# Kernel optimization log

Measured on AMD Instinct MI355X. Metric: run time of the kernel, lower is better.

Reference implementation:

```python
import jax, jax.numpy as jnp
import numpy as np

B, S, D = 4, 4096, 1024
E, I = 8, 2048
CAPACITY = 2
K = max(1, int(S / E * CAPACITY))  # tokens per expert per batch element


def setup_inputs() -> dict:
    key = jax.random.key(0)
    k1, k2, k3, k4, k5 = jax.random.split(key, 5)
    x = jax.random.normal(k1, (B, S, D), dtype=jnp.float32)
    gate_w = jax.random.normal(k2, (D, E), dtype=jnp.float32) * 0.006
    Wg = jax.random.normal(k3, (E, D, I), dtype=jnp.float32) * 0.02
    Wu = jax.random.normal(k4, (E, D, I), dtype=jnp.float32) * 0.02
    Wd = jax.random.normal(k5, (E, I, D), dtype=jnp.float32) * 0.02
    return {"x": x, "gate_w": gate_w, "Wg": Wg, "Wu": Wu, "Wd": Wd}


def reference(x, gate_w, Wg, Wu, Wd):
    # Router: softmax over experts per token, then per-expert top-k tokens.
    logits = jnp.einsum('bsd,de->bse', x, gate_w)          # [B,S,E]
    affinity = jax.nn.softmax(logits, axis=-1)
    affinity_T = jnp.transpose(affinity, (0, 2, 1))        # [B,E,S]
    gating, index = jax.lax.top_k(affinity_T, K)           # [B,E,K]

    # Gather selected tokens for all experts at once: [B,E,K,D]
    b_idx = jnp.arange(x.shape[0])[:, None, None]
    x_sel = x[b_idx, index]

    # Per-expert SwiGLU MLP (grouped GEMMs over the expert axis).
    g = jnp.einsum('bekd,edi->beki', x_sel, Wg)
    u = jnp.einsum('bekd,edi->beki', x_sel, Wu)
    h = jax.nn.silu(g) * u
    out = jnp.einsum('beki,eid->bekd', h, Wd)              # [B,E,K,D]

    # Weighted scatter-add combine back to token positions.
    contrib = out * gating[..., None]
    x_out = jnp.zeros_like(x).at[b_idx, index].add(contrib)
    return x_out
```

## Files before the change

### kernel.cpp

```cpp
#include <hip/hip_runtime.h>

#define B_ 4
#define S_ 4096
#define D_ 1024
#define E_ 8
#define I_ 2048
#define K_ 1024

typedef __attribute__((ext_vector_type(8))) short short8;
typedef __attribute__((ext_vector_type(4))) float f32x4;

__device__ __forceinline__ short f2bf(float f) {
  union { float f; unsigned u; } v; v.f = f;
  unsigned r = v.u + 0x7FFFu + ((v.u >> 16) & 1u);
  return (short)(r >> 16);
}

__device__ __forceinline__ void gload16(const void* g, void* l) {
  __builtin_amdgcn_global_load_lds((const __attribute__((address_space(1))) unsigned int*)g,
                                   (__attribute__((address_space(3))) unsigned int*)l, 16, 0, 0);
}

__global__ __launch_bounds__(256) void router_kernel(const float* __restrict__ x,
                                                     const float* __restrict__ gw,
                                                     double* __restrict__ affD) {
  int wave = threadIdx.x >> 6, lane = threadIdx.x & 63;
  int tok = blockIdx.x * 4 + wave;
  int b = tok >> 12, s = tok & (S_ - 1);
  const float* xr = x + (size_t)tok * D_;
  double acc[E_];
#pragma unroll
  for (int e = 0; e < E_; ++e) acc[e] = 0.0;
#pragma unroll 4
  for (int r = 0; r < 16; ++r) {
    int d = r * 64 + lane;
    float xv = xr[d];
    const float4* g4 = reinterpret_cast<const float4*>(gw + (size_t)d * E_);
    float4 g0 = g4[0], g1 = g4[1];
    acc[0] += (double)xv * g0.x; acc[1] += (double)xv * g0.y;
    acc[2] += (double)xv * g0.z; acc[3] += (double)xv * g0.w;
    acc[4] += (double)xv * g1.x; acc[5] += (double)xv * g1.y;
    acc[6] += (double)xv * g1.z; acc[7] += (double)xv * g1.w;
  }
#pragma unroll
  for (int off = 32; off > 0; off >>= 1) {
#pragma unroll
    for (int e = 0; e < E_; ++e) acc[e] += __shfl_xor(acc[e], off, 64);
  }
  double m = acc[0];
#pragma unroll
  for (int e = 1; e < E_; ++e) m = acc[e] > m ? acc[e] : m;
  double den = 0.0, ex[E_];
#pragma unroll
  for (int e = 0; e < E_; ++e) { ex[e] = exp(acc[e] - m); den += ex[e]; }
  if (lane < E_)
    affD[((size_t)b * E_ + lane) * S_ + s] = ex[lane] / den;
}

__global__ __launch_bounds__(1024) void topk_kernel(const double* __restrict__ affD,
                                                    int* __restrict__ idxArr,
                                                    float* __restrict__ gateArr) {
  __shared__ unsigned long long keys[S_];
  __shared__ int sidx[S_];
  int be = blockIdx.x, tid = threadIdx.x;
  const double* a = affD + (size_t)be * S_;
  for (int t = tid; t < S_; t += 1024) {
    keys[t] = (unsigned long long)__double_as_longlong(a[t]);
    sidx[t] = t;
  }
  __syncthreads();
  for (int k = 2; k <= S_; k <<= 1) {
    for (int j = k >> 1; j > 0; j >>= 1) {
      for (int t = tid; t < S_; t += 1024) {
        int x2 = t ^ j;
        if (x2 > t) {
          unsigned long long ka = keys[t], kb = keys[x2];
          int ia = sidx[t], ib = sidx[x2];
          bool agt = (ka > kb) || (ka == kb && ia < ib);
          bool up = ((t & k) == 0);
          if (up == agt) {
            keys[t] = kb; keys[x2] = ka;
            sidx[t] = ib; sidx[x2] = ia;
          }
        }
      }
      __syncthreads();
    }
  }
  for (int t = tid; t < K_; t += 1024) {
    int p = S_ - 1 - t;
    gateArr[(size_t)be * K_ + t] = (float)__longlong_as_double((long long)keys[p]);
    idxArr[(size_t)be * K_ + t] = sidx[p];
  }
}

__global__ __launch_bounds__(256) void transpose_cvt_kernel(const float* __restrict__ in,
                                                            unsigned short* __restrict__ out,
                                                            int M, int N) {
  __shared__ float t[64][65];
  int e = blockIdx.y;
  int ntn = N >> 6;
  int tm = (blockIdx.x / ntn) << 6;
  int tn = (blockIdx.x % ntn) << 6;
  const float* src = in + (size_t)e * M * N;
  unsigned short* dst = out + (size_t)e * M * N;
  int tid = threadIdx.x;
#pragma unroll
  for (int it = 0; it < 4; ++it) {
    int f = it * 256 + tid;
    int r = f >> 4, c4 = (f & 15) << 2;
    float4 v = *reinterpret_cast<const float4*>(&src[(size_t)(tm + r) * N + tn + c4]);
    t[c4][r] = v.x; t[c4 + 1][r] = v.y; t[c4 + 2][r] = v.z; t[c4 + 3][r] = v.w;
  }
  __syncthreads();
#pragma unroll
  for (int it = 0; it < 4; ++it) {
    int f = it * 256 + tid;
    int rr = f >> 4, c4 = (f & 15) << 2;
    short4 o;
    o.x = f2bf(t[rr][c4]); o.y = f2bf(t[rr][c4 + 1]);
    o.z = f2bf(t[rr][c4 + 2]); o.w = f2bf(t[rr][c4 + 3]);
    *reinterpret_cast<short4*>(&dst[(size_t)(tn + rr) * M + tm + c4]) = o;
  }
}

__global__ __launch_bounds__(256, 2) void mlp1_kernel(
    const float* __restrict__ x, const unsigned short* __restrict__ WgT,
    const unsigned short* __restrict__ WuT, const int* __restrict__ idxArr,
    unsigned short* __restrict__ H, int Ic, int i0) {
  const int Nt = Ic >> 7;
  int bid = blockIdx.x;
  int nt = bid % Nt; bid /= Nt;
  int mt = bid & 7; bid >>= 3;
  int be = bid;
  int b = be >> 3, e = be & 7;

  __shared__ short lsA[128 * 72];
  __shared__ short lsBg[128 * 64];
  __shared__ short lsBu[128 * 64];
  __shared__ int sTok[128];

  int tid = threadIdx.x;
  if (tid < 128) sTok[tid] = idxArr[(size_t)be * K_ + mt * 128 + tid];
  __syncthreads();

  const float* xb = x + (size_t)b * S_ * D_;
  const char* wg2 = (const char*)(WgT + (size_t)e * I_ * D_ + (size_t)(i0 + nt * 128) * D_);
  const char* wu2 = (const char*)(WuT + (size_t)e * I_ * D_ + (size_t)(i0 + nt * 128) * D_);

  int w = tid >> 6, lane = tid & 63;
  int wm = w >> 1, wn = w & 1;
  int lr = lane & 15, lg = lane >> 4;

  f32x4 accg[4][4], accu[4][4];
#pragma unroll
  for (int i = 0; i < 4; ++i)
#pragma unroll
    for (int j = 0; j < 4; ++j) {
      accg[i][j] = (f32x4){0.f, 0.f, 0.f, 0.f};
      accu[i][j] = (f32x4){0.f, 0.f, 0.f, 0.f};
    }

  for (int k0 = 0; k0 < D_; k0 += 64) {
#pragma unroll
    for (int c = 0; c < 4; ++c) {
      int flat = (c * 256 + tid) * 8;
      int row = flat >> 6, col = flat & 63;
      const float* src = xb + (size_t)sTok[row] * D_ + k0 + col;
      float4 f0 = *reinterpret_cast<const float4*>(src);
      float4 f1 = *reinterpret_cast<const float4*>(src + 4);
      short8 t;
      t[0] = f2bf(f0.x); t[1] = f2bf(f0.y); t[2] = f2bf(f0.z); t[3] = f2bf(f0.w);
      t[4] = f2bf(f1.x); t[5] = f2bf(f1.y); t[6] = f2bf(f1.z); t[7] = f2bf(f1.w);
      *reinterpret_cast<short8*>(&lsA[row * 72 + col]) = t;
    }
#pragma unroll
    for (int c = 0; c < 4; ++c) {
      int chunk = c * 4 + w;
      int fb = (chunk * 64 + lane) * 16;
      int row = fb >> 7, colb = fb & 127;
      size_t goff = (size_t)row * (D_ * 2) + (size_t)k0 * 2 + colb;
      gload16(wg2 + goff, (char*)lsBg + chunk * 1024);
      gload16(wu2 + goff, (char*)lsBu + chunk * 1024);
    }
    __syncthreads();
#pragma unroll
    for (int fk = 0; fk < 2; ++fk) {
      short8 af[4], bgf[4], buf[4];
#pragma unroll
      for (int fm = 0; fm < 4; ++fm)
        af[fm] = *reinterpret_cast<short8*>(&lsA[(wm * 64 + fm * 16 + lr) * 72 + fk * 32 + lg * 8]);
#pragma unroll
      for (int fn = 0; fn < 4; ++fn) {
        bgf[fn] = *reinterpret_cast<short8*>(&lsBg[(wn * 64 + fn * 16 + lr) * 64 + fk * 32 + lg * 8]);
        buf[fn] = *reinterpret_cast<short8*>(&lsBu[(wn * 64 + fn * 16 + lr) * 64 + fk * 32 + lg * 8]);
      }
#pragma unroll
      for (int fm = 0; fm < 4; ++fm)
#pragma unroll
        for (int fn = 0; fn < 4; ++fn) {
          accg[fm][fn] = __builtin_amdgcn_mfma_f32_16x16x32_bf16(af[fm], bgf[fn], accg[fm][fn], 0, 0, 0);
          accu[fm][fn] = __builtin_amdgcn_mfma_f32_16x16x32_bf16(af[fm], buf[fn], accu[fm][fn], 0, 0, 0);
        }
    }
    __syncthreads();
  }
  unsigned short* Hbe = H + (size_t)be * K_ * Ic;
#pragma unroll
  for (int fm = 0; fm < 4; ++fm)
#pragma unroll
    for (int fn = 0; fn < 4; ++fn) {
#pragma unroll
      for (int j = 0; j < 4; ++j) {
        float g = accg[fm][fn][j], u = accu[fm][fn][j];
        float h = g / (1.f + __expf(-g)) * u;
        int row = wm * 64 + fm * 16 + lg * 4 + j;
        int col = wn * 64 + fn * 16 + lr;
        Hbe[(size_t)(mt * 128 + row) * Ic + nt * 128 + col] = (unsigned short)f2bf(h);
      }
    }
}

__global__ __launch_bounds__(256, 2) void mlp2_kernel(
    const unsigned short* __restrict__ H, const unsigned short* __restrict__ WdT,
    const int* __restrict__ idxArr, const float* __restrict__ gateArr,
    float* __restrict__ out, int Ic, int i0) {
  int bid = blockIdx.x;
  int nt = bid & 7; bid >>= 3;
  int mt = bid & 7; bid >>= 3;
  int be = bid;
  int b = be >> 3, e = be & 7;

  __shared__ short lsA[128 * 64];
  __shared__ short lsB[128 * 64];
  __shared__ int sTok[128];
  __shared__ float sGate[128];

  int tid = threadIdx.x;
  if (tid < 128) {
    sTok[tid] = idxArr[(size_t)be * K_ + mt * 128 + tid];
    sGate[tid] = gateArr[(size_t)be * K_ + mt * 128 + tid];
  }
  __syncthreads();

  const char* Hbe = (const char*)(H + (size_t)be * K_ * Ic);
  const char* wd2 = (const char*)(WdT + (size_t)e * D_ * I_);

  int w = tid >> 6, lane = tid & 63;
  int wm = w >> 1, wn = w & 1;
  int lr = lane & 15, lg = lane >> 4;

  f32x4 acc[4][4];
#pragma unroll
  for (int i = 0; i < 4; ++i)
#pragma unroll
    for (int j = 0; j < 4; ++j) acc[i][j] = (f32x4){0.f, 0.f, 0.f, 0.f};

  for (int k0 = 0; k0 < Ic; k0 += 64) {
#pragma unroll
    for (int c = 0; c < 4; ++c) {
      int chunk = c * 4 + w;
      int fb = (chunk * 64 + lane) * 16;
      int row = fb >> 7, colb = fb & 127;
      gload16(Hbe + (size_t)(mt * 128 + row) * Ic * 2 + (size_t)k0 * 2 + colb,
              (char*)lsA + chunk * 1024);
      gload16(wd2 + ((size_t)(nt * 128 + row) * I_ + i0 + k0) * 2 + colb,
              (char*)lsB + chunk * 1024);
    }
    __syncthreads();
#pragma unroll
    for (int fk = 0; fk < 2; ++fk) {
      short8 af[4], bf[4];
#pragma unroll
      for (int fm = 0; fm < 4; ++fm)
        af[fm] = *reinterpret_cast<short8*>(&lsA[(wm * 64 + fm * 16 + lr) * 64 + fk * 32 + lg * 8]);
#pragma unroll
      for (int fn = 0; fn < 4; ++fn)
        bf[fn] = *reinterpret_cast<short8*>(&lsB[(wn * 64 + fn * 16 + lr) * 64 + fk * 32 + lg * 8]);
#pragma unroll
      for (int fm = 0; fm < 4; ++fm)
#pragma unroll
        for (int fn = 0; fn < 4; ++fn)
          acc[fm][fn] = __builtin_amdgcn_mfma_f32_16x16x32_bf16(af[fm], bf[fn], acc[fm][fn], 0, 0, 0);
    }
    __syncthreads();
  }
#pragma unroll
  for (int fm = 0; fm < 4; ++fm)
#pragma unroll
    for (int fn = 0; fn < 4; ++fn) {
#pragma unroll
      for (int j = 0; j < 4; ++j) {
        int row = wm * 64 + fm * 16 + lg * 4 + j;
        int col = nt * 128 + wn * 64 + fn * 16 + lr;
        float v = acc[fm][fn][j] * sGate[row];
        atomicAdd(&out[((size_t)b * S_ + sTok[row]) * D_ + col], v);
      }
    }
}

extern "C" void kernel_launch(void* const* d_in, const int* in_sizes, int n_in,
                              void* d_out, int out_size, void* d_ws, size_t ws_size,
                              hipStream_t stream) {
  const float* x  = (const float*)d_in[0];
  const float* gw = (const float*)d_in[1];
  const float* Wg = (const float*)d_in[2];
  const float* Wu = (const float*)d_in[3];
  const float* Wd = (const float*)d_in[4];
  float* out = (float*)d_out;
  char* ws = (char*)d_ws;

  size_t off = 0;
  double* affD = (double*)(ws + off); off += (size_t)B_ * E_ * S_ * sizeof(double);
  int* idxArr = (int*)(ws + off);     off += (size_t)B_ * E_ * K_ * sizeof(int);
  float* gateArr = (float*)(ws + off); off += (size_t)B_ * E_ * K_ * sizeof(float);
  off = (off + 255) & ~(size_t)255;
  unsigned short* WgT = (unsigned short*)(ws + off); off += (size_t)E_ * D_ * I_ * 2;
  unsigned short* WuT = (unsigned short*)(ws + off); off += (size_t)E_ * D_ * I_ * 2;
  unsigned short* WdT = (unsigned short*)(ws + off); off += (size_t)E_ * D_ * I_ * 2;
  off = (off + 255) & ~(size_t)255;
  unsigned short* H = (unsigned short*)(ws + off);
  size_t rem = (ws_size > off) ? (ws_size - off) : 0;

  int Ic = 128;
  for (int c = I_; c >= 128; c >>= 1) {
    if ((size_t)B_ * E_ * K_ * (size_t)c * 2 <= rem) { Ic = c; break; }
  }

  hipMemsetAsync(d_out, 0, (size_t)out_size * sizeof(float), stream);
  router_kernel<<<B_ * S_ / 4, 256, 0, stream>>>(x, gw, affD);
  topk_kernel<<<B_ * E_, 1024, 0, stream>>>(affD, idxArr, gateArr);
  transpose_cvt_kernel<<<dim3((D_ / 64) * (I_ / 64), E_), 256, 0, stream>>>(Wg, WgT, D_, I_);
  transpose_cvt_kernel<<<dim3((D_ / 64) * (I_ / 64), E_), 256, 0, stream>>>(Wu, WuT, D_, I_);
  transpose_cvt_kernel<<<dim3((I_ / 64) * (D_ / 64), E_), 256, 0, stream>>>(Wd, WdT, I_, D_);
  for (int i0 = 0; i0 < I_; i0 += Ic) {
    mlp1_kernel<<<B_ * E_ * 8 * (Ic / 128), 256, 0, stream>>>(x, WgT, WuT, idxArr, H, Ic, i0);
    mlp2_kernel<<<B_ * E_ * 8 * 8, 256, 0, stream>>>(H, WdT, idxArr, gateArr, out, Ic, i0);
  }
}
```

Before: 805.4 us.

## Pre-gather bf16 tokens, swizzle LDS tiles, and remap workgroups across XCDs

Adds a gather kernel that converts the selected tokens to a contiguous bf16 buffer. mlp1 can then load A tiles with direct global-to-LDS loads instead of doing per-iteration fp32 gathers and conversions. Both MLP kernels now use an XOR-swizzled LDS layout in place of padding to avoid bank conflicts, and remap block IDs so neighbouring tiles land on the same XCD for L2 reuse. This costs an extra kernel launch and about 64 MB of workspace, which can shrink the available Ic chunk size.

```diff
diff --git a/kernel.cpp b/kernel.cpp
--- a/kernel.cpp
+++ b/kernel.cpp
@@ -19,6 +19,11 @@
 __device__ __forceinline__ void gload16(const void* g, void* l) {
   __builtin_amdgcn_global_load_lds((const __attribute__((address_space(1))) unsigned int*)g,
                                    (__attribute__((address_space(3))) unsigned int*)l, 16, 0, 0);
+}
+
+__device__ __forceinline__ short8 rdswz(const short* ls, int row, int cb) {
+  int byte = (row << 7) + (cb ^ ((row & 7) << 4));
+  return *reinterpret_cast<const short8*>(reinterpret_cast<const char*>(ls) + byte);
 }
 
 __global__ __launch_bounds__(256) void router_kernel(const float* __restrict__ x,
@@ -124,33 +129,51 @@
   }
 }
 
+__global__ __launch_bounds__(256) void gather_cvt_kernel(const float* __restrict__ x,
+                                                         const int* __restrict__ idxArr,
+                                                         unsigned short* __restrict__ Xsel) {
+  int row = blockIdx.x * 4 + (threadIdx.x >> 6);
+  int lane = threadIdx.x & 63;
+  int b = row >> 13;
+  int tok = idxArr[row];
+  const float* src = x + ((size_t)b * S_ + tok) * D_;
+  unsigned short* dst = Xsel + (size_t)row * D_;
+#pragma unroll
+  for (int it = 0; it < 4; ++it) {
+    int d = it * 256 + lane * 4;
+    float4 v = *reinterpret_cast<const float4*>(src + d);
+    short4 o;
+    o.x = f2bf(v.x); o.y = f2bf(v.y); o.z = f2bf(v.z); o.w = f2bf(v.w);
+    *reinterpret_cast<short4*>(dst + d) = o;
+  }
+}
+
 __global__ __launch_bounds__(256, 2) void mlp1_kernel(
-    const float* __restrict__ x, const unsigned short* __restrict__ WgT,
-    const unsigned short* __restrict__ WuT, const int* __restrict__ idxArr,
-    unsigned short* __restrict__ H, int Ic, int i0) {
+    const unsigned short* __restrict__ Xsel, const unsigned short* __restrict__ WgT,
+    const unsigned short* __restrict__ WuT, unsigned short* __restrict__ H,
+    int Ic, int i0) {
   const int Nt = Ic >> 7;
-  int bid = blockIdx.x;
+  int nwg = gridDim.x;
+  int bid = (blockIdx.x & 7) * (nwg >> 3) + (blockIdx.x >> 3);
   int nt = bid % Nt; bid /= Nt;
   int mt = bid & 7; bid >>= 3;
   int be = bid;
-  int b = be >> 3, e = be & 7;
-
-  __shared__ short lsA[128 * 72];
+  int e = be & 7;
+
+  __shared__ short lsA[128 * 64];
   __shared__ short lsBg[128 * 64];
   __shared__ short lsBu[128 * 64];
-  __shared__ int sTok[128];
-
-  int tid = threadIdx.x;
-  if (tid < 128) sTok[tid] = idxArr[(size_t)be * K_ + mt * 128 + tid];
-  __syncthreads();
-
-  const float* xb = x + (size_t)b * S_ * D_;
-  const char* wg2 = (const char*)(WgT + (size_t)e * I_ * D_ + (size_t)(i0 + nt * 128) * D_);
-  const char* wu2 = (const char*)(WuT + (size_t)e * I_ * D_ + (size_t)(i0 + nt * 128) * D_);
-
-  int w = tid >> 6, lane = tid & 63;
+
+  int tid = threadIdx.x, w = tid >> 6, lane = tid & 63;
   int wm = w >> 1, wn = w & 1;
   int lr = lane & 15, lg = lane >> 4;
+
+  const char* pa = (const char*)(Xsel + ((size_t)be * K_ + mt * 128) * D_);
+  const char* pg = (const char*)(WgT + (size_t)e * I_ * D_ + (size_t)(i0 + nt * 128) * D_);
+  const char* pu = (const char*)(WuT + (size_t)e * I_ * D_ + (size_t)(i0 + nt * 128) * D_);
+
+  int srow = lane >> 3;
+  int scol = ((lane & 7) ^ srow) << 4;
 
   f32x4 accg[4][4], accu[4][4];
 #pragma unroll
@@ -164,36 +187,25 @@
   for (int k0 = 0; k0 < D_; k0 += 64) {
 #pragma unroll
     for (int c = 0; c < 4; ++c) {
-      int flat = (c * 256 + tid) * 8;
-      int row = flat >> 6, col = flat & 63;
-      const float* src = xb + (size_t)sTok[row] * D_ + k0 + col;
-      float4 f0 = *reinterpret_cast<const float4*>(src);
-      float4 f1 = *reinterpret_cast<const float4*>(src + 4);
-      short8 t;
-      t[0] = f2bf(f0.x); t[1] = f2bf(f0.y); t[2] = f2bf(f0.z); t[3] = f2bf(f0.w);
-      t[4] = f2bf(f1.x); t[5] = f2bf(f1.y); t[6] = f2bf(f1.z); t[7] = f2bf(f1.w);
-      *reinterpret_cast<short8*>(&lsA[row * 72 + col]) = t;
-    }
-#pragma unroll
-    for (int c = 0; c < 4; ++c) {
       int chunk = c * 4 + w;
-      int fb = (chunk * 64 + lane) * 16;
-      int row = fb >> 7, colb = fb & 127;
-      size_t goff = (size_t)row * (D_ * 2) + (size_t)k0 * 2 + colb;
-      gload16(wg2 + goff, (char*)lsBg + chunk * 1024);
-      gload16(wu2 + goff, (char*)lsBu + chunk * 1024);
+      int row = chunk * 8 + srow;
+      size_t go = (size_t)row * (D_ * 2) + (size_t)k0 * 2 + scol;
+      gload16(pa + go, (char*)lsA + chunk * 1024);
+      gload16(pg + go, (char*)lsBg + chunk * 1024);
+      gload16(pu + go, (char*)lsBu + chunk * 1024);
     }
     __syncthreads();
 #pragma unroll
     for (int fk = 0; fk < 2; ++fk) {
+      int cb = fk * 64 + lg * 16;
       short8 af[4], bgf[4], buf[4];
 #pragma unroll
       for (int fm = 0; fm < 4; ++fm)
-        af[fm] = *reinterpret_cast<short8*>(&lsA[(wm * 64 + fm * 16 + lr) * 72 + fk * 32 + lg * 8]);
+        af[fm] = rdswz(lsA, wm * 64 + fm * 16 + lr, cb);
 #pragma unroll
       for (int fn = 0; fn < 4; ++fn) {
-        bgf[fn] = *reinterpret_cast<short8*>(&lsBg[(wn * 64 + fn * 16 + lr) * 64 + fk * 32 + lg * 8]);
-        buf[fn] = *reinterpret_cast<short8*>(&lsBu[(wn * 64 + fn * 16 + lr) * 64 + fk * 32 + lg * 8]);
+        bgf[fn] = rdswz(lsBg, wn * 64 + fn * 16 + lr, cb);
+        buf[fn] = rdswz(lsBu, wn * 64 + fn * 16 + lr, cb);
       }
 #pragma unroll
       for (int fm = 0; fm < 4; ++fm)
@@ -225,7 +237,8 @@
     const unsigned short* __restrict__ H, const unsigned short* __restrict__ WdT,
     const int* __restrict__ idxArr, const float* __restrict__ gateArr,
     float* __restrict__ out, int Ic, int i0) {
-  int bid = blockIdx.x;
+  int nwg = gridDim.x;
+  int bid = (blockIdx.x & 7) * (nwg >> 3) + (blockIdx.x >> 3);
   int nt = bid & 7; bid >>= 3;
   int mt = bid & 7; bid >>= 3;
   int be = bid;
@@ -241,15 +254,17 @@
     sTok[tid] = idxArr[(size_t)be * K_ + mt * 128 + tid];
     sGate[tid] = gateArr[(size_t)be * K_ + mt * 128 + tid];
   }
-  __syncthreads();
-
-  const char* Hbe = (const char*)(H + (size_t)be * K_ * Ic);
-  const char* wd2 = (const char*)(WdT + (size_t)e * D_ * I_);
+
+  const char* pa = (const char*)(H + ((size_t)be * K_ + mt * 128) * Ic);
+  const char* pb = (const char*)(WdT + (size_t)e * D_ * I_ + (size_t)(nt * 128) * I_ + i0);
 
   int w = tid >> 6, lane = tid & 63;
   int wm = w >> 1, wn = w & 1;
   int lr = lane & 15, lg = lane >> 4;
 
+  int srow = lane >> 3;
+  int scol = ((lane & 7) ^ srow) << 4;
+
   f32x4 acc[4][4];
 #pragma unroll
   for (int i = 0; i < 4; ++i)
@@ -260,23 +275,21 @@
 #pragma unroll
     for (int c = 0; c < 4; ++c) {
       int chunk = c * 4 + w;
-      int fb = (chunk * 64 + lane) * 16;
-      int row = fb >> 7, colb = fb & 127;
-      gload16(Hbe + (size_t)(mt * 128 + row) * Ic * 2 + (size_t)k0 * 2 + colb,
-              (char*)lsA + chunk * 1024);
-      gload16(wd2 + ((size_t)(nt * 128 + row) * I_ + i0 + k0) * 2 + colb,
-              (char*)lsB + chunk * 1024);
+      int row = chunk * 8 + srow;
+      gload16(pa + (size_t)row * (Ic * 2) + (size_t)k0 * 2 + scol, (char*)lsA + chunk * 1024);
+      gload16(pb + (size_t)row * (I_ * 2) + (size_t)k0 * 2 + scol, (char*)lsB + chunk * 1024);
     }
     __syncthreads();
 #pragma unroll
     for (int fk = 0; fk < 2; ++fk) {
+      int cb = fk * 64 + lg * 16;
       short8 af[4], bf[4];
 #pragma unroll
       for (int fm = 0; fm < 4; ++fm)
-        af[fm] = *reinterpret_cast<short8*>(&lsA[(wm * 64 + fm * 16 + lr) * 64 + fk * 32 + lg * 8]);
+        af[fm] = rdswz(lsA, wm * 64 + fm * 16 + lr, cb);
 #pragma unroll
       for (int fn = 0; fn < 4; ++fn)
-        bf[fn] = *reinterpret_cast<short8*>(&lsB[(wn * 64 + fn * 16 + lr) * 64 + fk * 32 + lg * 8]);
+        bf[fn] = rdswz(lsB, wn * 64 + fn * 16 + lr, cb);
 #pragma unroll
       for (int fm = 0; fm < 4; ++fm)
 #pragma unroll
@@ -318,6 +331,7 @@
   unsigned short* WgT = (unsigned short*)(ws + off); off += (size_t)E_ * D_ * I_ * 2;
   unsigned short* WuT = (unsigned short*)(ws + off); off += (size_t)E_ * D_ * I_ * 2;
   unsigned short* WdT = (unsigned short*)(ws + off); off += (size_t)E_ * D_ * I_ * 2;
+  unsigned short* Xsel = (unsigned short*)(ws + off); off += (size_t)B_ * E_ * K_ * D_ * 2;
   off = (off + 255) & ~(size_t)255;
   unsigned short* H = (unsigned short*)(ws + off);
   size_t rem = (ws_size > off) ? (ws_size - off) : 0;
@@ -333,8 +347,9 @@
   transpose_cvt_kernel<<<dim3((D_ / 64) * (I_ / 64), E_), 256, 0, stream>>>(Wg, WgT, D_, I_);
   transpose_cvt_kernel<<<dim3((D_ / 64) * (I_ / 64), E_), 256, 0, stream>>>(Wu, WuT, D_, I_);
   transpose_cvt_kernel<<<dim3((I_ / 64) * (D_ / 64), E_), 256, 0, stream>>>(Wd, WdT, I_, D_);
+  gather_cvt_kernel<<<B_ * E_ * K_ / 4, 256, 0, stream>>>(x, idxArr, Xsel);
   for (int i0 = 0; i0 < I_; i0 += Ic) {
-    mlp1_kernel<<<B_ * E_ * 8 * (Ic / 128), 256, 0, stream>>>(x, WgT, WuT, idxArr, H, Ic, i0);
+    mlp1_kernel<<<B_ * E_ * 8 * (Ic / 128), 256, 0, stream>>>(Xsel, WgT, WuT, H, Ic, i0);
     mlp2_kernel<<<B_ * E_ * 8 * 8, 256, 0, stream>>>(H, WdT, idxArr, gateArr, out, Ic, i0);
   }
 }
```

Result: no change. 801.2 us (-0.5%).
